# Kernel tuning notes

Hardware: AMD Instinct MI355X
Metric: run time of the kernel (lower is better)

Reference implementation:

```python
import jax, jax.numpy as jnp
import numpy as np

NUM_EXPERTS = 8
TOP_K = 2
N_EMBD = 1024
D_FFN = 2048  # 4*n_embd//top_k, already multiple of block_size=128


def setup_inputs() -> dict:
    key = jax.random.key(0)
    k1, k2, k3, k4 = jax.random.split(key, 4)
    x = jax.random.normal(k1, (4, 2048, N_EMBD), dtype=jnp.float32)
    router_w = jax.random.normal(k2, (NUM_EXPERTS, N_EMBD), dtype=jnp.float32) * 0.02
    w1 = jax.random.normal(k3, (N_EMBD, D_FFN * NUM_EXPERTS), dtype=jnp.float32) * 0.02
    w2 = jax.random.normal(k4, (D_FFN * NUM_EXPERTS, N_EMBD), dtype=jnp.float32) * 0.02
    return {"x": x, "router_w": router_w, "w1": w1, "w2": w2}


def reference(x, router_w, w1, w2):
    B, T, D = x.shape
    xf = x.reshape(B * T, D)                       # [N, d]
    N = B * T

    # Router: softmax over experts, then top-k selection and renormalization.
    logits = xf @ router_w.T                       # [N, E]
    probs = jax.nn.softmax(logits, axis=-1)
    top_v, top_i = jax.lax.top_k(probs, TOP_K)     # [N, k]
    top_v = top_v / jnp.sum(top_v, axis=-1, keepdims=True)  # norm_topk_prob=True

    # Dense [N, E] routing-weight matrix (zero for non-selected experts).
    gate = jnp.zeros((N, NUM_EXPERTS), dtype=x.dtype)
    gate = gate.at[jnp.arange(N)[:, None], top_i].set(top_v)

    w1r = w1.reshape(D, NUM_EXPERTS, D_FFN)        # expert-major column blocks
    w2r = w2.reshape(NUM_EXPERTS, D_FFN, D)

    out = jnp.zeros((N, D), dtype=x.dtype)
    for e in range(NUM_EXPERTS):
        h = jax.nn.gelu(xf @ w1r[:, e, :], approximate=False)  # [N, f]
        out = out + gate[:, e:e + 1] * (h @ w2r[e])
    return out.reshape(B, T, D)
```

## Files before the change

kernel.cpp:

```cpp
#include <hip/hip_runtime.h>
#include <hip/hip_bf16.h>
#include <cstdint>
#include <cstddef>

#define NE 8
#define N_TOK 8192
#define D_EMB 1024
#define D_FFN 2048

#define BM 128
#define BN 128
#define BK 32

typedef __attribute__((ext_vector_type(8))) short short8;
typedef __attribute__((ext_vector_type(4))) float f32x4;

__device__ __forceinline__ unsigned short f2bf(float f) {
  union { float f; unsigned int u; } c; c.f = f;
  unsigned int u = c.u;
  unsigned int r = u + 0x7FFFu + ((u >> 16) & 1u);
  return (unsigned short)(r >> 16);
}

__device__ __forceinline__ float bf2f(unsigned short u) {
  union { unsigned int u; float f; } c; c.u = ((unsigned int)u) << 16;
  return c.f;
}

__device__ __forceinline__ void gll16(const void* g, void* l) {
  __builtin_amdgcn_global_load_lds((const __attribute__((address_space(1))) void*)g,
                                   (__attribute__((address_space(3))) void*)l, 16, 0, 0);
}

__global__ __launch_bounds__(256) void router_k(const float* __restrict__ x,
                                                const float* __restrict__ rw,
                                                int* __restrict__ ti,
                                                float* __restrict__ tg,
                                                ushort* __restrict__ xb) {
  int w = threadIdx.x >> 6, lane = threadIdx.x & 63;
  int n = blockIdx.x * 4 + w;
  const float4* x4 = (const float4*)(x + (size_t)n * D_EMB);
  ushort4* xb4 = (ushort4*)(xb + (size_t)n * D_EMB);
  const float4* r4 = (const float4*)rw;
  float acc[NE];
#pragma unroll
  for (int e = 0; e < NE; ++e) acc[e] = 0.f;
#pragma unroll
  for (int c = 0; c < 4; ++c) {
    float4 xv = x4[c * 64 + lane];
    ushort4 o;
    o.x = f2bf(xv.x); o.y = f2bf(xv.y); o.z = f2bf(xv.z); o.w = f2bf(xv.w);
    xb4[c * 64 + lane] = o;
#pragma unroll
    for (int e = 0; e < NE; ++e) {
      float4 wv = r4[e * 256 + c * 64 + lane];
      acc[e] += xv.x * wv.x + xv.y * wv.y + xv.z * wv.z + xv.w * wv.w;
    }
  }
#pragma unroll
  for (int e = 0; e < NE; ++e) {
    float v = acc[e];
#pragma unroll
    for (int off = 32; off >= 1; off >>= 1) v += __shfl_xor(v, off);
    acc[e] = v;
  }
  if (lane == 0) {
    int e0 = 0; float v0 = acc[0];
#pragma unroll
    for (int e = 1; e < NE; ++e) if (acc[e] > v0) { v0 = acc[e]; e0 = e; }
    int e1 = -1; float v1 = -1e30f;
#pragma unroll
    for (int e = 0; e < NE; ++e) if (e != e0 && acc[e] > v1) { v1 = acc[e]; e1 = e; }
    float p1 = expf(v1 - v0);
    float g0 = 1.f / (1.f + p1);
    float g1 = p1 * g0;
    ti[2 * n] = e0; ti[2 * n + 1] = e1;
    tg[2 * n] = g0; tg[2 * n + 1] = g1;
  }
}

__global__ __launch_bounds__(256) void hist_k(const int* __restrict__ ti,
                                              int* __restrict__ counts) {
  __shared__ int lc[NE];
  if (threadIdx.x < NE) lc[threadIdx.x] = 0;
  __syncthreads();
  int s = blockIdx.x * 512 + threadIdx.x;
  atomicAdd(&lc[ti[s]], 1);
  atomicAdd(&lc[ti[s + 256]], 1);
  __syncthreads();
  if (threadIdx.x < NE) atomicAdd(&counts[threadIdx.x], lc[threadIdx.x]);
}

__global__ void prefix_k(const int* __restrict__ counts, int* __restrict__ bases,
                         int* __restrict__ cursor) {
  if (threadIdx.x == 0) {
    int s = 0;
    for (int e = 0; e < NE; ++e) { bases[e] = s; cursor[e] = s; s += counts[e]; }
  }
}

__global__ __launch_bounds__(256) void scatter_k(const int* __restrict__ ti,
                                                 const float* __restrict__ tg,
                                                 int* __restrict__ cursor,
                                                 int* __restrict__ tok,
                                                 float* __restrict__ gate,
                                                 int* __restrict__ inv) {
  __shared__ int lc[NE], lb[NE];
  if (threadIdx.x < NE) lc[threadIdx.x] = 0;
  __syncthreads();
  int s = blockIdx.x * 256 + threadIdx.x;
  int e = ti[s];
  float g = tg[s];
  int loc = atomicAdd(&lc[e], 1);
  __syncthreads();
  if (threadIdx.x < NE) lb[threadIdx.x] = atomicAdd(&cursor[threadIdx.x], lc[threadIdx.x]);
  __syncthreads();
  int pos = lb[e] + loc;
  tok[pos] = s >> 1;
  gate[pos] = g;
  inv[s] = pos;
}

__global__ __launch_bounds__(256) void transpose_bf_k(const float* __restrict__ src,
                                                      ushort* __restrict__ dst,
                                                      int R, int C) {
  __shared__ ushort t[32][33];
  int bx = blockIdx.x, by = blockIdx.y;
  int rl = threadIdx.x >> 3, q = threadIdx.x & 7;
  float4 v = *(const float4*)&src[(size_t)(by * 32 + rl) * C + bx * 32 + q * 4];
  t[rl][q * 4 + 0] = f2bf(v.x);
  t[rl][q * 4 + 1] = f2bf(v.y);
  t[rl][q * 4 + 2] = f2bf(v.z);
  t[rl][q * 4 + 3] = f2bf(v.w);
  __syncthreads();
  ushort4 o;
  o.x = t[q * 4 + 0][rl];
  o.y = t[q * 4 + 1][rl];
  o.z = t[q * 4 + 2][rl];
  o.w = t[q * 4 + 3][rl];
  *(ushort4*)&dst[(size_t)(bx * 32 + rl) * R + by * 32 + q * 4] = o;
}


__global__ __launch_bounds__(256) void gemm1_k(const ushort* __restrict__ xb,
                                               const ushort* __restrict__ w1t,
                                               const int* __restrict__ counts,
                                               const int* __restrict__ bases,
                                               const int* __restrict__ tok,
                                               ushort* __restrict__ h) {
  int bid = (int)blockIdx.x;
  bid = (bid & 7) * (NE * 1024 / 8) + (bid >> 3);
  int e = bid >> 10;
  int rem = bid & 1023;
  int mt = rem >> 4, nt = rem & 15;
  int count = counts[e];
  if (mt * BM >= count) return;
  int base = bases[e];

  __shared__ ushort Al[BM * BK];
  __shared__ ushort Bl[BN * BK];

  int tid = threadIdx.x;
  int w = tid >> 6, lane = tid & 63;

  const int ssw = (((lane & 3) ^ ((lane >> 3) & 3))) * 8;

  const ushort* aptr[2]; const ushort* bptr[2];
  ushort* alds[2]; ushort* blds[2];
#pragma unroll
  for (int j = 0; j < 2; ++j) {
    int rl = w * 32 + j * 16 + (lane >> 2);
    int pr = min(base + mt * BM + rl, base + count - 1);
    int t = tok[pr];
    aptr[j] = xb + (size_t)t * D_EMB + ssw;
    int c = e * D_FFN + nt * BN + rl;
    bptr[j] = w1t + (size_t)c * D_EMB + ssw;
    alds[j] = Al + (w * 32 + j * 16) * BK;
    blds[j] = Bl + (w * 32 + j * 16) * BK;
  }

  f32x4 zero = {0.f, 0.f, 0.f, 0.f};
  f32x4 acc[4][4];
#pragma unroll
  for (int i = 0; i < 4; ++i)
#pragma unroll
    for (int j = 0; j < 4; ++j) acc[i][j] = zero;

  int wm = w >> 1, wn = w & 1;
  const int rsw = ((lane >> 4) ^ (((lane & 15) >> 1) & 3)) * 8;
  const int arow = (wm * 64 + (lane & 15)) * BK + rsw;
  const int brow = (wn * 64 + (lane & 15)) * BK + rsw;

  for (int ks = 0; ks < D_EMB / BK; ++ks) {
    __syncthreads();
#pragma unroll
    for (int j = 0; j < 2; ++j) {
      gll16(aptr[j], alds[j]);
      gll16(bptr[j], blds[j]);
      aptr[j] += BK; bptr[j] += BK;
    }
    __syncthreads();
    short8 a[4], b[4];
#pragma unroll
    for (int i = 0; i < 4; ++i) a[i] = *(const short8*)&Al[arow + i * 16 * BK];
#pragma unroll
    for (int j = 0; j < 4; ++j) b[j] = *(const short8*)&Bl[brow + j * 16 * BK];
#pragma unroll
    for (int i = 0; i < 4; ++i)
#pragma unroll
      for (int j = 0; j < 4; ++j)
        acc[i][j] = __builtin_amdgcn_mfma_f32_16x16x32_bf16(a[i], b[j], acc[i][j], 0, 0, 0);
  }

  int r0 = mt * BM + wm * 64, c0 = nt * BN + wn * 64;
#pragma unroll
  for (int i = 0; i < 4; ++i) {
#pragma unroll
    for (int q = 0; q < 4; ++q) {
      int row = r0 + i * 16 + (lane >> 4) * 4 + q;
      if (row < count) {
        size_t hb = (size_t)(base + row) * D_FFN;
#pragma unroll
        for (int j = 0; j < 4; ++j) {
          float v = acc[i][j][q];
          v = 0.5f * v * (1.f + erff(v * 0.70710678118654752f));
          h[hb + c0 + j * 16 + (lane & 15)] = f2bf(v);
        }
      }
    }
  }
}

__global__ __launch_bounds__(256) void gemm2_k(const ushort* __restrict__ h,
                                               const ushort* __restrict__ w2t,
                                               const int* __restrict__ counts,
                                               const int* __restrict__ bases,
                                               const int* __restrict__ tok,
                                               const float* __restrict__ gate,
                                               ushort* __restrict__ y) {
  int bid = (int)blockIdx.x;
  bid = (bid & 7) * (NE * 512 / 8) + (bid >> 3);
  int e = bid >> 9;
  int rem = bid & 511;
  int mt = rem >> 3, nt = rem & 7;
  int count = counts[e];
  if (mt * BM >= count) return;
  int base = bases[e];

  __shared__ ushort Al[BM * BK];
  __shared__ ushort Bl[BN * BK];

  int tid = threadIdx.x;
  int w = tid >> 6, lane = tid & 63;

  const int ssw = (((lane & 3) ^ ((lane >> 3) & 3))) * 8;

  const ushort* aptr[2]; const ushort* bptr[2];
  ushort* alds[2]; ushort* blds[2];
#pragma unroll
  for (int j = 0; j < 2; ++j) {
    int rl = w * 32 + j * 16 + (lane >> 2);
    int pr = min(base + mt * BM + rl, base + count - 1);
    aptr[j] = h + (size_t)pr * D_FFN + ssw;
    int d = nt * BN + rl;
    bptr[j] = w2t + (size_t)d * (NE * D_FFN) + e * D_FFN + ssw;
    alds[j] = Al + (w * 32 + j * 16) * BK;
    blds[j] = Bl + (w * 32 + j * 16) * BK;
  }

  f32x4 zero = {0.f, 0.f, 0.f, 0.f};
  f32x4 acc[4][4];
#pragma unroll
  for (int i = 0; i < 4; ++i)
#pragma unroll
    for (int j = 0; j < 4; ++j) acc[i][j] = zero;

  int wm = w >> 1, wn = w & 1;
  const int rsw = ((lane >> 4) ^ (((lane & 15) >> 1) & 3)) * 8;
  const int arow = (wm * 64 + (lane & 15)) * BK + rsw;
  const int brow = (wn * 64 + (lane & 15)) * BK + rsw;

  for (int ks = 0; ks < D_FFN / BK; ++ks) {
    __syncthreads();
#pragma unroll
    for (int j = 0; j < 2; ++j) {
      gll16(aptr[j], alds[j]);
      gll16(bptr[j], blds[j]);
      aptr[j] += BK; bptr[j] += BK;
    }
    __syncthreads();
    short8 a[4], b[4];
#pragma unroll
    for (int i = 0; i < 4; ++i) a[i] = *(const short8*)&Al[arow + i * 16 * BK];
#pragma unroll
    for (int j = 0; j < 4; ++j) b[j] = *(const short8*)&Bl[brow + j * 16 * BK];
#pragma unroll
    for (int i = 0; i < 4; ++i)
#pragma unroll
      for (int j = 0; j < 4; ++j)
        acc[i][j] = __builtin_amdgcn_mfma_f32_16x16x32_bf16(a[i], b[j], acc[i][j], 0, 0, 0);
  }

  int r0 = mt * BM + wm * 64, c0 = nt * BN + wn * 64;
#pragma unroll
  for (int i = 0; i < 4; ++i) {
#pragma unroll
    for (int q = 0; q < 4; ++q) {
      int row = r0 + i * 16 + (lane >> 4) * 4 + q;
      if (row < count) {
        int pr = base + row;
        float g = gate[pr];
        size_t yb = (size_t)pr * D_EMB;
#pragma unroll
        for (int j = 0; j < 4; ++j) {
          y[yb + c0 + j * 16 + (lane & 15)] = f2bf(g * acc[i][j][q]);
        }
      }
    }
  }
}

__global__ __launch_bounds__(256) void combine_k(const ushort* __restrict__ y,
                                                 const int* __restrict__ inv,
                                                 float* __restrict__ out) {
  int n = blockIdx.x;
  int p0 = inv[2 * n], p1 = inv[2 * n + 1];
  const ushort4* r0 = (const ushort4*)(y + (size_t)p0 * D_EMB);
  const ushort4* r1 = (const ushort4*)(y + (size_t)p1 * D_EMB);
  float4* o = (float4*)(out + (size_t)n * D_EMB);
  int i = threadIdx.x;
  ushort4 a = r0[i], b = r1[i];
  float4 v;
  v.x = bf2f(a.x) + bf2f(b.x);
  v.y = bf2f(a.y) + bf2f(b.y);
  v.z = bf2f(a.z) + bf2f(b.z);
  v.w = bf2f(a.w) + bf2f(b.w);
  o[i] = v;
}

extern "C" void kernel_launch(void* const* d_in, const int* in_sizes, int n_in,
                              void* d_out, int out_size, void* d_ws, size_t ws_size,
                              hipStream_t stream) {
  const float* x  = (const float*)d_in[0];
  const float* rw = (const float*)d_in[1];
  const float* w1 = (const float*)d_in[2];
  const float* w2 = (const float*)d_in[3];
  float* out = (float*)d_out;

  char* ws = (char*)d_ws;
  size_t off = 0;
  auto alloc = [&](size_t bytes) {
    void* p = ws + off;
    off = (off + bytes + 255) & ~(size_t)255;
    return p;
  };
  int*    counts = (int*)alloc(32);
  int*    bases  = (int*)alloc(32);
  int*    cursor = (int*)alloc(32);
  int*    ti     = (int*)alloc((size_t)N_TOK * 2 * sizeof(int));
  float*  tg     = (float*)alloc((size_t)N_TOK * 2 * sizeof(float));
  int*    tok    = (int*)alloc((size_t)N_TOK * 2 * sizeof(int));
  float*  gate   = (float*)alloc((size_t)N_TOK * 2 * sizeof(float));
  int*    inv    = (int*)alloc((size_t)N_TOK * 2 * sizeof(int));
  ushort* xb     = (ushort*)alloc((size_t)N_TOK * D_EMB * 2);
  ushort* w1t    = (ushort*)alloc((size_t)D_EMB * NE * D_FFN * 2);
  ushort* w2t    = (ushort*)alloc((size_t)D_EMB * NE * D_FFN * 2);
  ushort* hbuf   = (ushort*)alloc((size_t)N_TOK * 2 * D_FFN * 2);
  ushort* ybuf   = (ushort*)alloc((size_t)N_TOK * 2 * D_EMB * 2);
  (void)ws_size; (void)in_sizes; (void)n_in; (void)out_size;

  hipMemsetAsync(counts, 0, 32, stream);

  router_k<<<N_TOK / 4, 256, 0, stream>>>(x, rw, ti, tg, xb);
  transpose_bf_k<<<dim3(512, 32), 256, 0, stream>>>(w1, w1t, D_EMB, NE * D_FFN);
  transpose_bf_k<<<dim3(32, 512), 256, 0, stream>>>(w2, w2t, NE * D_FFN, D_EMB);
  hist_k<<<N_TOK * 2 / 512, 256, 0, stream>>>(ti, counts);
  prefix_k<<<1, 64, 0, stream>>>(counts, bases, cursor);
  scatter_k<<<N_TOK * 2 / 256, 256, 0, stream>>>(ti, tg, cursor, tok, gate, inv);
  gemm1_k<<<NE * 64 * 16, 256, 0, stream>>>(xb, w1t, counts, bases, tok, hbuf);
  gemm2_k<<<NE * 64 * 8, 256, 0, stream>>>(hbuf, w2t, counts, bases, tok, gate, ybuf);
  combine_k<<<N_TOK, 256, 0, stream>>>(ybuf, inv, out);
}
```

Baseline: 284.6 us.

## Double-buffer LDS tiles in both expert GEMMs to overlap loads with MFMA

```diff
diff --git a/kernel.cpp b/kernel.cpp
--- a/kernel.cpp
+++ b/kernel.cpp
@@ -140,6 +140,7 @@
   o.w = t[q * 4 + 3][rl];
   *(ushort4*)&dst[(size_t)(bx * 32 + rl) * R + by * 32 + q * 4] = o;
 }
+
 
 
 __global__ __launch_bounds__(256) void gemm1_k(const ushort* __restrict__ xb,
@@ -157,8 +158,8 @@
   if (mt * BM >= count) return;
   int base = bases[e];
 
-  __shared__ ushort Al[BM * BK];
-  __shared__ ushort Bl[BN * BK];
+  __shared__ ushort Al[2][BM * BK];
+  __shared__ ushort Bl[2][BN * BK];
 
   int tid = threadIdx.x;
   int w = tid >> 6, lane = tid & 63;
@@ -166,7 +167,7 @@
   const int ssw = (((lane & 3) ^ ((lane >> 3) & 3))) * 8;
 
   const ushort* aptr[2]; const ushort* bptr[2];
-  ushort* alds[2]; ushort* blds[2];
+  int ldso[2];
 #pragma unroll
   for (int j = 0; j < 2; ++j) {
     int rl = w * 32 + j * 16 + (lane >> 2);
@@ -175,8 +176,7 @@
     aptr[j] = xb + (size_t)t * D_EMB + ssw;
     int c = e * D_FFN + nt * BN + rl;
     bptr[j] = w1t + (size_t)c * D_EMB + ssw;
-    alds[j] = Al + (w * 32 + j * 16) * BK;
-    blds[j] = Bl + (w * 32 + j * 16) * BK;
+    ldso[j] = (w * 32 + j * 16) * BK;
   }
 
   f32x4 zero = {0.f, 0.f, 0.f, 0.f};
@@ -191,26 +191,39 @@
   const int arow = (wm * 64 + (lane & 15)) * BK + rsw;
   const int brow = (wn * 64 + (lane & 15)) * BK + rsw;
 
-  for (int ks = 0; ks < D_EMB / BK; ++ks) {
-    __syncthreads();
-#pragma unroll
-    for (int j = 0; j < 2; ++j) {
-      gll16(aptr[j], alds[j]);
-      gll16(bptr[j], blds[j]);
-      aptr[j] += BK; bptr[j] += BK;
-    }
-    __syncthreads();
-    short8 a[4], b[4];
-#pragma unroll
-    for (int i = 0; i < 4; ++i) a[i] = *(const short8*)&Al[arow + i * 16 * BK];
-#pragma unroll
-    for (int j = 0; j < 4; ++j) b[j] = *(const short8*)&Bl[brow + j * 16 * BK];
-#pragma unroll
-    for (int i = 0; i < 4; ++i)
-#pragma unroll
-      for (int j = 0; j < 4; ++j)
-        acc[i][j] = __builtin_amdgcn_mfma_f32_16x16x32_bf16(a[i], b[j], acc[i][j], 0, 0, 0);
-  }
+#define STAGE1(BUF)                                         \
+  {                                                         \
+    _Pragma("unroll")                                       \
+    for (int j = 0; j < 2; ++j) {                           \
+      gll16(aptr[j], &Al[BUF][ldso[j]]);                    \
+      gll16(bptr[j], &Bl[BUF][ldso[j]]);                    \
+      aptr[j] += BK; bptr[j] += BK;                         \
+    }                                                       \
+  }
+#define COMPUTE1(BUF)                                       \
+  {                                                         \
+    short8 a[4], b[4];                                      \
+    _Pragma("unroll")                                       \
+    for (int i = 0; i < 4; ++i) a[i] = *(const short8*)&Al[BUF][arow + i * 16 * BK]; \
+    _Pragma("unroll")                                       \
+    for (int j = 0; j < 4; ++j) b[j] = *(const short8*)&Bl[BUF][brow + j * 16 * BK]; \
+    _Pragma("unroll")                                       \
+    for (int i = 0; i < 4; ++i)                             \
+      _Pragma("unroll")                                     \
+      for (int j = 0; j < 4; ++j)                           \
+        acc[i][j] = __builtin_amdgcn_mfma_f32_16x16x32_bf16(a[i], b[j], acc[i][j], 0, 0, 0); \
+  }
+
+  STAGE1(0);
+  __syncthreads();
+  for (int ks = 0; ks < (D_EMB / BK) - 2; ks += 2) {
+    STAGE1(1); COMPUTE1(0); __syncthreads();
+    STAGE1(0); COMPUTE1(1); __syncthreads();
+  }
+  STAGE1(1); COMPUTE1(0); __syncthreads();
+  COMPUTE1(1);
+#undef STAGE1
+#undef COMPUTE1
 
   int r0 = mt * BM + wm * 64, c0 = nt * BN + wn * 64;
 #pragma unroll
@@ -247,8 +260,8 @@
   if (mt * BM >= count) return;
   int base = bases[e];
 
-  __shared__ ushort Al[BM * BK];
-  __shared__ ushort Bl[BN * BK];
+  __shared__ ushort Al[2][BM * BK];
+  __shared__ ushort Bl[2][BN * BK];
 
   int tid = threadIdx.x;
   int w = tid >> 6, lane = tid & 63;
@@ -256,7 +269,7 @@
   const int ssw = (((lane & 3) ^ ((lane >> 3) & 3))) * 8;
 
   const ushort* aptr[2]; const ushort* bptr[2];
-  ushort* alds[2]; ushort* blds[2];
+  int ldso[2];
 #pragma unroll
   for (int j = 0; j < 2; ++j) {
     int rl = w * 32 + j * 16 + (lane >> 2);
@@ -264,8 +277,7 @@
     aptr[j] = h + (size_t)pr * D_FFN + ssw;
     int d = nt * BN + rl;
     bptr[j] = w2t + (size_t)d * (NE * D_FFN) + e * D_FFN + ssw;
-    alds[j] = Al + (w * 32 + j * 16) * BK;
-    blds[j] = Bl + (w * 32 + j * 16) * BK;
+    ldso[j] = (w * 32 + j * 16) * BK;
   }
 
   f32x4 zero = {0.f, 0.f, 0.f, 0.f};
@@ -280,26 +292,39 @@
   const int arow = (wm * 64 + (lane & 15)) * BK + rsw;
   const int brow = (wn * 64 + (lane & 15)) * BK + rsw;
 
-  for (int ks = 0; ks < D_FFN / BK; ++ks) {
-    __syncthreads();
-#pragma unroll
-    for (int j = 0; j < 2; ++j) {
-      gll16(aptr[j], alds[j]);
-      gll16(bptr[j], blds[j]);
-      aptr[j] += BK; bptr[j] += BK;
-    }
-    __syncthreads();
-    short8 a[4], b[4];
-#pragma unroll
-    for (int i = 0; i < 4; ++i) a[i] = *(const short8*)&Al[arow + i * 16 * BK];
-#pragma unroll
-    for (int j = 0; j < 4; ++j) b[j] = *(const short8*)&Bl[brow + j * 16 * BK];
-#pragma unroll
-    for (int i = 0; i < 4; ++i)
-#pragma unroll
-      for (int j = 0; j < 4; ++j)
-        acc[i][j] = __builtin_amdgcn_mfma_f32_16x16x32_bf16(a[i], b[j], acc[i][j], 0, 0, 0);
-  }
+#define STAGE2(BUF)                                         \
+  {                                                         \
+    _Pragma("unroll")                                       \
+    for (int j = 0; j < 2; ++j) {                           \
+      gll16(aptr[j], &Al[BUF][ldso[j]]);                    \
+      gll16(bptr[j], &Bl[BUF][ldso[j]]);                    \
+      aptr[j] += BK; bptr[j] += BK;                         \
+    }                                                       \
+  }
+#define COMPUTE2(BUF)                                       \
+  {                                                         \
+    short8 a[4], b[4];                                      \
+    _Pragma("unroll")                                       \
+    for (int i = 0; i < 4; ++i) a[i] = *(const short8*)&Al[BUF][arow + i * 16 * BK]; \
+    _Pragma("unroll")                                       \
+    for (int j = 0; j < 4; ++j) b[j] = *(const short8*)&Bl[BUF][brow + j * 16 * BK]; \
+    _Pragma("unroll")                                       \
+    for (int i = 0; i < 4; ++i)                             \
+      _Pragma("unroll")                                     \
+      for (int j = 0; j < 4; ++j)                           \
+        acc[i][j] = __builtin_amdgcn_mfma_f32_16x16x32_bf16(a[i], b[j], acc[i][j], 0, 0, 0); \
+  }
+
+  STAGE2(0);
+  __syncthreads();
+  for (int ks = 0; ks < (D_FFN / BK) - 2; ks += 2) {
+    STAGE2(1); COMPUTE2(0); __syncthreads();
+    STAGE2(0); COMPUTE2(1); __syncthreads();
+  }
+  STAGE2(1); COMPUTE2(0); __syncthreads();
+  COMPUTE2(1);
+#undef STAGE2
+#undef COMPUTE2
 
   int r0 = mt * BM + wm * 64, c0 = nt * BN + wn * 64;
 #pragma unroll
```

After: 303.5 us. +6.6%, slower.

## Rewrite expert GEMMs as 256x256 double-buffered 8-wave tiles with interleaved MFMA

Applied to the files above, without the earlier changes.

```diff
diff --git a/kernel.cpp b/kernel.cpp
--- a/kernel.cpp
+++ b/kernel.cpp
@@ -7,10 +7,6 @@
 #define N_TOK 8192
 #define D_EMB 1024
 #define D_FFN 2048
-
-#define BM 128
-#define BN 128
-#define BK 32
 
 typedef __attribute__((ext_vector_type(8))) short short8;
 typedef __attribute__((ext_vector_type(4))) float f32x4;
@@ -31,6 +27,8 @@
   __builtin_amdgcn_global_load_lds((const __attribute__((address_space(1))) void*)g,
                                    (__attribute__((address_space(3))) void*)l, 16, 0, 0);
 }
+
+#define SB() __builtin_amdgcn_sched_barrier(0)
 
 __global__ __launch_bounds__(256) void router_k(const float* __restrict__ x,
                                                 const float* __restrict__ rw,
@@ -142,79 +140,117 @@
 }
 
 
-__global__ __launch_bounds__(256) void gemm1_k(const ushort* __restrict__ xb,
-                                               const ushort* __restrict__ w1t,
-                                               const int* __restrict__ counts,
-                                               const int* __restrict__ bases,
-                                               const int* __restrict__ tok,
-                                               ushort* __restrict__ h) {
+#define RD_A(dst, BASE, ROFF)                                              \
+  { _Pragma("unroll") for (int f_ = 0; f_ < 4; ++f_)                       \
+    _Pragma("unroll") for (int kk_ = 0; kk_ < 2; ++kk_) {                  \
+      int row_ = (ROFF) + f_ * 16 + (lane & 15);                           \
+      int s_ = kk_ * 4 + (lane >> 4);                                      \
+      dst[f_][kk_] = *(const short8*)&(BASE)[row_ * 64 + ((s_ ^ (row_ & 7)) * 8)]; \
+    } }
+
+#define RD_B(dst, BASE, ROFF)                                              \
+  { _Pragma("unroll") for (int g_ = 0; g_ < 2; ++g_)                       \
+    _Pragma("unroll") for (int kk_ = 0; kk_ < 2; ++kk_) {                  \
+      int row_ = (ROFF) + g_ * 16 + (lane & 15);                           \
+      int s_ = kk_ * 4 + (lane >> 4);                                      \
+      dst[g_][kk_] = *(const short8*)&(BASE)[row_ * 64 + ((s_ ^ (row_ & 7)) * 8)]; \
+    } }
+
+#define MFMA_Q(QR, QC, FA, FB)                                             \
+  { __builtin_amdgcn_s_setprio(1);                                        \
+    _Pragma("unroll") for (int f_ = 0; f_ < 4; ++f_)                       \
+    _Pragma("unroll") for (int g_ = 0; g_ < 2; ++g_)                       \
+    _Pragma("unroll") for (int kk_ = 0; kk_ < 2; ++kk_)                    \
+      acc[(QR) * 4 + f_][(QC) * 2 + g_] = __builtin_amdgcn_mfma_f32_16x16x32_bf16( \
+          FA[f_][kk_], FB[g_][kk_], acc[(QR) * 4 + f_][(QC) * 2 + g_], 0, 0, 0);   \
+    __builtin_amdgcn_s_setprio(0); }
+
+#define STAGE(AD, BD)                                                      \
+  { _Pragma("unroll") for (int r_ = 0; r_ < 4; ++r_) {                     \
+      gll16(aP[r_], (AD) + (r_ * 64 + wv * 8) * 64); aP[r_] += 64;         \
+      gll16(bP[r_], (BD) + (r_ * 64 + wv * 8) * 64); bP[r_] += 64;         \
+    } }
+
+#define TILE(CURA, CURB, NXTA, NXTB, DONXT)                                \
+  {                                                                \
+    if (DONXT) { STAGE(NXTA, NXTB); }                                      \
+    RD_A(fA1, CURA, wm * 128 + 64); RD_B(fB1, CURB, wn * 64 + 32);         \
+    MFMA_Q(0, 0, fA0, fB0);                                                \
+    SB(); __builtin_amdgcn_s_barrier(); SB();                              \
+                                                                   \
+    MFMA_Q(0, 1, fA0, fB1);                                                \
+    SB(); __builtin_amdgcn_s_barrier(); SB();                              \
+                                                                   \
+    MFMA_Q(1, 0, fA1, fB0);                                                \
+    SB(); __builtin_amdgcn_s_barrier(); SB();                              \
+                                                                   \
+    MFMA_Q(1, 1, fA1, fB1);                                                \
+    if (DONXT) { asm volatile("s_waitcnt vmcnt(0)" ::: "memory"); SB(); }  \
+    SB(); __builtin_amdgcn_s_barrier(); SB();                              \
+    if (DONXT) { RD_A(fA0, NXTA, wm * 128); RD_B(fB0, NXTB, wn * 64); }    \
+  }
+
+__global__ __launch_bounds__(512, 2) void gemm1_k(const ushort* __restrict__ xb,
+                                                  const ushort* __restrict__ w1t,
+                                                  const int* __restrict__ counts,
+                                                  const int* __restrict__ bases,
+                                                  const int* __restrict__ tok,
+                                                  ushort* __restrict__ h) {
   int bid = (int)blockIdx.x;
-  bid = (bid & 7) * (NE * 1024 / 8) + (bid >> 3);
-  int e = bid >> 10;
-  int rem = bid & 1023;
-  int mt = rem >> 4, nt = rem & 15;
+  bid = (bid & 7) * 256 + (bid >> 3);
+  int e = bid >> 8;
+  int rem = bid & 255;
+  int mt = rem >> 3, nt = rem & 7;
   int count = counts[e];
-  if (mt * BM >= count) return;
+  if (mt * 256 >= count) return;
   int base = bases[e];
 
-  __shared__ ushort Al[BM * BK];
-  __shared__ ushort Bl[BN * BK];
+  extern __shared__ ushort smem[];
+  ushort* A0_ = smem;
+  ushort* A1_ = smem + 16384;
+  ushort* B0_ = smem + 32768;
+  ushort* B1_ = smem + 49152;
 
   int tid = threadIdx.x;
-  int w = tid >> 6, lane = tid & 63;
-
-  const int ssw = (((lane & 3) ^ ((lane >> 3) & 3))) * 8;
-
-  const ushort* aptr[2]; const ushort* bptr[2];
-  ushort* alds[2]; ushort* blds[2];
-#pragma unroll
-  for (int j = 0; j < 2; ++j) {
-    int rl = w * 32 + j * 16 + (lane >> 2);
-    int pr = min(base + mt * BM + rl, base + count - 1);
+  int wv = tid >> 6, lane = tid & 63;
+  int wm = wv >> 2, wn = wv & 3;
+  const int swc = ((tid & 7) ^ ((tid >> 3) & 7)) * 8;
+
+  const ushort* aP[4]; const ushort* bP[4];
+#pragma unroll
+  for (int r = 0; r < 4; ++r) {
+    int row = mt * 256 + r * 64 + (tid >> 3);
+    int pr = min(base + row, base + count - 1);
     int t = tok[pr];
-    aptr[j] = xb + (size_t)t * D_EMB + ssw;
-    int c = e * D_FFN + nt * BN + rl;
-    bptr[j] = w1t + (size_t)c * D_EMB + ssw;
-    alds[j] = Al + (w * 32 + j * 16) * BK;
-    blds[j] = Bl + (w * 32 + j * 16) * BK;
+    aP[r] = xb + (size_t)t * D_EMB + swc;
+    int cB = e * D_FFN + nt * 256 + r * 64 + (tid >> 3);
+    bP[r] = w1t + (size_t)cB * D_EMB + swc;
   }
 
   f32x4 zero = {0.f, 0.f, 0.f, 0.f};
-  f32x4 acc[4][4];
-#pragma unroll
-  for (int i = 0; i < 4; ++i)
+  f32x4 acc[8][4];
+#pragma unroll
+  for (int i = 0; i < 8; ++i)
 #pragma unroll
     for (int j = 0; j < 4; ++j) acc[i][j] = zero;
 
-  int wm = w >> 1, wn = w & 1;
-  const int rsw = ((lane >> 4) ^ (((lane & 15) >> 1) & 3)) * 8;
-  const int arow = (wm * 64 + (lane & 15)) * BK + rsw;
-  const int brow = (wn * 64 + (lane & 15)) * BK + rsw;
-
-  for (int ks = 0; ks < D_EMB / BK; ++ks) {
-    __syncthreads();
-#pragma unroll
-    for (int j = 0; j < 2; ++j) {
-      gll16(aptr[j], alds[j]);
-      gll16(bptr[j], blds[j]);
-      aptr[j] += BK; bptr[j] += BK;
-    }
-    __syncthreads();
-    short8 a[4], b[4];
-#pragma unroll
-    for (int i = 0; i < 4; ++i) a[i] = *(const short8*)&Al[arow + i * 16 * BK];
-#pragma unroll
-    for (int j = 0; j < 4; ++j) b[j] = *(const short8*)&Bl[brow + j * 16 * BK];
-#pragma unroll
-    for (int i = 0; i < 4; ++i)
-#pragma unroll
-      for (int j = 0; j < 4; ++j)
-        acc[i][j] = __builtin_amdgcn_mfma_f32_16x16x32_bf16(a[i], b[j], acc[i][j], 0, 0, 0);
-  }
-
-  int r0 = mt * BM + wm * 64, c0 = nt * BN + wn * 64;
-#pragma unroll
-  for (int i = 0; i < 4; ++i) {
+  short8 fA0[4][2], fA1[4][2], fB0[2][2], fB1[2][2];
+
+  STAGE(A0_, B0_);
+  asm volatile("s_waitcnt vmcnt(0)" ::: "memory"); SB();
+  __builtin_amdgcn_s_barrier(); SB();
+  RD_A(fA0, A0_, wm * 128); RD_B(fB0, B0_, wn * 64);
+
+  const int NT = D_EMB / 64;
+  for (int tp = 0; tp < NT / 2; ++tp) {
+    TILE(A0_, B0_, A1_, B1_, 1);
+    int dn = (tp != NT / 2 - 1);
+    TILE(A1_, B1_, A0_, B0_, dn);
+  }
+
+  int r0 = mt * 256 + wm * 128, c0 = nt * 256 + wn * 64;
+#pragma unroll
+  for (int i = 0; i < 8; ++i) {
 #pragma unroll
     for (int q = 0; q < 4; ++q) {
       int row = r0 + i * 16 + (lane >> 4) * 4 + q;
@@ -231,79 +267,66 @@
   }
 }
 
-__global__ __launch_bounds__(256) void gemm2_k(const ushort* __restrict__ h,
-                                               const ushort* __restrict__ w2t,
-                                               const int* __restrict__ counts,
-                                               const int* __restrict__ bases,
-                                               const int* __restrict__ tok,
-                                               const float* __restrict__ gate,
-                                               ushort* __restrict__ y) {
+__global__ __launch_bounds__(512, 2) void gemm2_k(const ushort* __restrict__ h,
+                                                  const ushort* __restrict__ w2t,
+                                                  const int* __restrict__ counts,
+                                                  const int* __restrict__ bases,
+                                                  const float* __restrict__ gate,
+                                                  ushort* __restrict__ y) {
   int bid = (int)blockIdx.x;
-  bid = (bid & 7) * (NE * 512 / 8) + (bid >> 3);
-  int e = bid >> 9;
-  int rem = bid & 511;
-  int mt = rem >> 3, nt = rem & 7;
+  bid = (bid & 7) * 128 + (bid >> 3);
+  int e = bid >> 7;
+  int rem = bid & 127;
+  int mt = rem >> 2, nt = rem & 3;
   int count = counts[e];
-  if (mt * BM >= count) return;
+  if (mt * 256 >= count) return;
   int base = bases[e];
 
-  __shared__ ushort Al[BM * BK];
-  __shared__ ushort Bl[BN * BK];
+  extern __shared__ ushort smem[];
+  ushort* A0_ = smem;
+  ushort* A1_ = smem + 16384;
+  ushort* B0_ = smem + 32768;
+  ushort* B1_ = smem + 49152;
 
   int tid = threadIdx.x;
-  int w = tid >> 6, lane = tid & 63;
-
-  const int ssw = (((lane & 3) ^ ((lane >> 3) & 3))) * 8;
-
-  const ushort* aptr[2]; const ushort* bptr[2];
-  ushort* alds[2]; ushort* blds[2];
-#pragma unroll
-  for (int j = 0; j < 2; ++j) {
-    int rl = w * 32 + j * 16 + (lane >> 2);
-    int pr = min(base + mt * BM + rl, base + count - 1);
-    aptr[j] = h + (size_t)pr * D_FFN + ssw;
-    int d = nt * BN + rl;
-    bptr[j] = w2t + (size_t)d * (NE * D_FFN) + e * D_FFN + ssw;
-    alds[j] = Al + (w * 32 + j * 16) * BK;
-    blds[j] = Bl + (w * 32 + j * 16) * BK;
+  int wv = tid >> 6, lane = tid & 63;
+  int wm = wv >> 2, wn = wv & 3;
+  const int swc = ((tid & 7) ^ ((tid >> 3) & 7)) * 8;
+
+  const ushort* aP[4]; const ushort* bP[4];
+#pragma unroll
+  for (int r = 0; r < 4; ++r) {
+    int row = mt * 256 + r * 64 + (tid >> 3);
+    int pr = min(base + row, base + count - 1);
+    aP[r] = h + (size_t)pr * D_FFN + swc;
+    int cB = nt * 256 + r * 64 + (tid >> 3);
+    bP[r] = w2t + (size_t)cB * (NE * D_FFN) + e * D_FFN + swc;
   }
 
   f32x4 zero = {0.f, 0.f, 0.f, 0.f};
-  f32x4 acc[4][4];
-#pragma unroll
-  for (int i = 0; i < 4; ++i)
+  f32x4 acc[8][4];
+#pragma unroll
+  for (int i = 0; i < 8; ++i)
 #pragma unroll
     for (int j = 0; j < 4; ++j) acc[i][j] = zero;
 
-  int wm = w >> 1, wn = w & 1;
-  const int rsw = ((lane >> 4) ^ (((lane & 15) >> 1) & 3)) * 8;
-  const int arow = (wm * 64 + (lane & 15)) * BK + rsw;
-  const int brow = (wn * 64 + (lane & 15)) * BK + rsw;
-
-  for (int ks = 0; ks < D_FFN / BK; ++ks) {
-    __syncthreads();
-#pragma unroll
-    for (int j = 0; j < 2; ++j) {
-      gll16(aptr[j], alds[j]);
-      gll16(bptr[j], blds[j]);
-      aptr[j] += BK; bptr[j] += BK;
-    }
-    __syncthreads();
-    short8 a[4], b[4];
-#pragma unroll
-    for (int i = 0; i < 4; ++i) a[i] = *(const short8*)&Al[arow + i * 16 * BK];
-#pragma unroll
-    for (int j = 0; j < 4; ++j) b[j] = *(const short8*)&Bl[brow + j * 16 * BK];
-#pragma unroll
-    for (int i = 0; i < 4; ++i)
-#pragma unroll
-      for (int j = 0; j < 4; ++j)
-        acc[i][j] = __builtin_amdgcn_mfma_f32_16x16x32_bf16(a[i], b[j], acc[i][j], 0, 0, 0);
-  }
-
-  int r0 = mt * BM + wm * 64, c0 = nt * BN + wn * 64;
-#pragma unroll
-  for (int i = 0; i < 4; ++i) {
+  short8 fA0[4][2], fA1[4][2], fB0[2][2], fB1[2][2];
+
+  STAGE(A0_, B0_);
+  asm volatile("s_waitcnt vmcnt(0)" ::: "memory"); SB();
+  __builtin_amdgcn_s_barrier(); SB();
+  RD_A(fA0, A0_, wm * 128); RD_B(fB0, B0_, wn * 64);
+
+  const int NT = D_FFN / 64;
+  for (int tp = 0; tp < NT / 2; ++tp) {
+    TILE(A0_, B0_, A1_, B1_, 1);
+    int dn = (tp != NT / 2 - 1);
+    TILE(A1_, B1_, A0_, B0_, dn);
+  }
+
+  int r0 = mt * 256 + wm * 128, c0 = nt * 256 + wn * 64;
+#pragma unroll
+  for (int i = 0; i < 8; ++i) {
 #pragma unroll
     for (int q = 0; q < 4; ++q) {
       int row = r0 + i * 16 + (lane >> 4) * 4 + q;
@@ -369,6 +392,9 @@
   ushort* ybuf   = (ushort*)alloc((size_t)N_TOK * 2 * D_EMB * 2);
   (void)ws_size; (void)in_sizes; (void)n_in; (void)out_size;
 
+  hipFuncSetAttribute((const void*)gemm1_k, hipFuncAttributeMaxDynamicSharedMemorySize, 131072);
+  hipFuncSetAttribute((const void*)gemm2_k, hipFuncAttributeMaxDynamicSharedMemorySize, 131072);
+
   hipMemsetAsync(counts, 0, 32, stream);
 
   router_k<<<N_TOK / 4, 256, 0, stream>>>(x, rw, ti, tg, xb);
@@ -377,7 +403,7 @@
   hist_k<<<N_TOK * 2 / 512, 256, 0, stream>>>(ti, counts);
   prefix_k<<<1, 64, 0, stream>>>(counts, bases, cursor);
   scatter_k<<<N_TOK * 2 / 256, 256, 0, stream>>>(ti, tg, cursor, tok, gate, inv);
-  gemm1_k<<<NE * 64 * 16, 256, 0, stream>>>(xb, w1t, counts, bases, tok, hbuf);
-  gemm2_k<<<NE * 64 * 8, 256, 0, stream>>>(hbuf, w2t, counts, bases, tok, gate, ybuf);
+  gemm1_k<<<NE * 256, 512, 131072, stream>>>(xb, w1t, counts, bases, tok, hbuf);
+  gemm2_k<<<NE * 128, 512, 131072, stream>>>(hbuf, w2t, counts, bases, gate, ybuf);
   combine_k<<<N_TOK, 256, 0, stream>>>(ybuf, inv, out);
 }
```

After: 413.8 us. 1.45x slower.

## Double-buffer LDS with BK=64 and async-load pipelining in expert GEMMs

Applied to the files above, without the earlier changes.

```diff
diff --git a/kernel.cpp b/kernel.cpp
--- a/kernel.cpp
+++ b/kernel.cpp
@@ -10,7 +10,7 @@
 
 #define BM 128
 #define BN 128
-#define BK 32
+#define BK 64
 
 typedef __attribute__((ext_vector_type(8))) short short8;
 typedef __attribute__((ext_vector_type(4))) float f32x4;
@@ -31,6 +31,10 @@
   __builtin_amdgcn_global_load_lds((const __attribute__((address_space(1))) void*)g,
                                    (__attribute__((address_space(3))) void*)l, 16, 0, 0);
 }
+
+#define SB() __builtin_amdgcn_sched_barrier(0)
+#define VW(N) { asm volatile("s_waitcnt vmcnt(" #N ")" ::: "memory"); SB(); }
+#define BAR() { SB(); __builtin_amdgcn_s_barrier(); SB(); }
 
 __global__ __launch_bounds__(256) void router_k(const float* __restrict__ x,
                                                 const float* __restrict__ rw,
@@ -141,6 +145,39 @@
   *(ushort4*)&dst[(size_t)(bx * 32 + rl) * R + by * 32 + q * 4] = o;
 }
 
+
+#define STAGEK(BUF)                                                        \
+  { _Pragma("unroll") for (int r_ = 0; r_ < 4; ++r_) {                     \
+      gll16(aP[r_], &Al[BUF][r_ * 2048 + w * 512]); aP[r_] += BK;          \
+      gll16(bP[r_], &Bl[BUF][r_ * 2048 + w * 512]); bP[r_] += BK;          \
+    } }
+
+#define COMPUTEK(BUF)                                                      \
+  { short8 a[4], b[4];                                                     \
+    _Pragma("unroll") for (int i = 0; i < 4; ++i)                          \
+      a[i] = *(const short8*)&Al[BUF][(wm * 64 + i * 16 + l15) * 64 + q0]; \
+    _Pragma("unroll") for (int j = 0; j < 4; ++j)                          \
+      b[j] = *(const short8*)&Bl[BUF][(wn * 64 + j * 16 + l15) * 64 + q0]; \
+    _Pragma("unroll") for (int i = 0; i < 4; ++i)                          \
+      _Pragma("unroll") for (int j = 0; j < 4; ++j)                        \
+        acc[i][j] = __builtin_amdgcn_mfma_f32_16x16x32_bf16(a[i], b[j], acc[i][j], 0, 0, 0); \
+    _Pragma("unroll") for (int i = 0; i < 4; ++i)                          \
+      a[i] = *(const short8*)&Al[BUF][(wm * 64 + i * 16 + l15) * 64 + (q0 ^ 32)]; \
+    _Pragma("unroll") for (int j = 0; j < 4; ++j)                          \
+      b[j] = *(const short8*)&Bl[BUF][(wn * 64 + j * 16 + l15) * 64 + (q0 ^ 32)]; \
+    _Pragma("unroll") for (int i = 0; i < 4; ++i)                          \
+      _Pragma("unroll") for (int j = 0; j < 4; ++j)                        \
+        acc[i][j] = __builtin_amdgcn_mfma_f32_16x16x32_bf16(a[i], b[j], acc[i][j], 0, 0, 0); \
+  }
+
+#define KLOOP(NT)                                                          \
+  STAGEK(0);                                                               \
+  for (int ks = 0; ks < (NT) - 2; ks += 2) {                               \
+    STAGEK(1); VW(8); BAR(); COMPUTEK(0); BAR();                           \
+    STAGEK(0); VW(8); BAR(); COMPUTEK(1); BAR();                           \
+  }                                                                        \
+  STAGEK(1); VW(8); BAR(); COMPUTEK(0); BAR();                             \
+  VW(0); BAR(); COMPUTEK(1);
 
 __global__ __launch_bounds__(256) void gemm1_k(const ushort* __restrict__ xb,
                                                const ushort* __restrict__ w1t,
@@ -157,26 +194,25 @@
   if (mt * BM >= count) return;
   int base = bases[e];
 
-  __shared__ ushort Al[BM * BK];
-  __shared__ ushort Bl[BN * BK];
+  __shared__ ushort Al[2][BM * BK];
+  __shared__ ushort Bl[2][BN * BK];
 
   int tid = threadIdx.x;
   int w = tid >> 6, lane = tid & 63;
-
-  const int ssw = (((lane & 3) ^ ((lane >> 3) & 3))) * 8;
-
-  const ushort* aptr[2]; const ushort* bptr[2];
-  ushort* alds[2]; ushort* blds[2];
-#pragma unroll
-  for (int j = 0; j < 2; ++j) {
-    int rl = w * 32 + j * 16 + (lane >> 2);
-    int pr = min(base + mt * BM + rl, base + count - 1);
+  const int l15 = lane & 15;
+  const int q0 = (((lane >> 4) ^ (lane & 7))) * 8;
+
+  const int swc = (((tid & 7) ^ ((tid >> 3) & 7))) * 8;
+
+  const ushort* aP[4]; const ushort* bP[4];
+#pragma unroll
+  for (int r = 0; r < 4; ++r) {
+    int R = r * 32 + (tid >> 3);
+    int pr = min(base + mt * BM + R, base + count - 1);
     int t = tok[pr];
-    aptr[j] = xb + (size_t)t * D_EMB + ssw;
-    int c = e * D_FFN + nt * BN + rl;
-    bptr[j] = w1t + (size_t)c * D_EMB + ssw;
-    alds[j] = Al + (w * 32 + j * 16) * BK;
-    blds[j] = Bl + (w * 32 + j * 16) * BK;
+    aP[r] = xb + (size_t)t * D_EMB + swc;
+    int cB = e * D_FFN + nt * BN + R;
+    bP[r] = w1t + (size_t)cB * D_EMB + swc;
   }
 
   f32x4 zero = {0.f, 0.f, 0.f, 0.f};
@@ -187,30 +223,8 @@
     for (int j = 0; j < 4; ++j) acc[i][j] = zero;
 
   int wm = w >> 1, wn = w & 1;
-  const int rsw = ((lane >> 4) ^ (((lane & 15) >> 1) & 3)) * 8;
-  const int arow = (wm * 64 + (lane & 15)) * BK + rsw;
-  const int brow = (wn * 64 + (lane & 15)) * BK + rsw;
-
-  for (int ks = 0; ks < D_EMB / BK; ++ks) {
-    __syncthreads();
-#pragma unroll
-    for (int j = 0; j < 2; ++j) {
-      gll16(aptr[j], alds[j]);
-      gll16(bptr[j], blds[j]);
-      aptr[j] += BK; bptr[j] += BK;
-    }
-    __syncthreads();
-    short8 a[4], b[4];
-#pragma unroll
-    for (int i = 0; i < 4; ++i) a[i] = *(const short8*)&Al[arow + i * 16 * BK];
-#pragma unroll
-    for (int j = 0; j < 4; ++j) b[j] = *(const short8*)&Bl[brow + j * 16 * BK];
-#pragma unroll
-    for (int i = 0; i < 4; ++i)
-#pragma unroll
-      for (int j = 0; j < 4; ++j)
-        acc[i][j] = __builtin_amdgcn_mfma_f32_16x16x32_bf16(a[i], b[j], acc[i][j], 0, 0, 0);
-  }
+
+  KLOOP(D_EMB / BK);
 
   int r0 = mt * BM + wm * 64, c0 = nt * BN + wn * 64;
 #pragma unroll
@@ -224,7 +238,7 @@
         for (int j = 0; j < 4; ++j) {
           float v = acc[i][j][q];
           v = 0.5f * v * (1.f + erff(v * 0.70710678118654752f));
-          h[hb + c0 + j * 16 + (lane & 15)] = f2bf(v);
+          h[hb + c0 + j * 16 + l15] = f2bf(v);
         }
       }
     }
@@ -235,7 +249,6 @@
                                                const ushort* __restrict__ w2t,
                                                const int* __restrict__ counts,
                                                const int* __restrict__ bases,
-                                               const int* __restrict__ tok,
                                                const float* __restrict__ gate,
                                                ushort* __restrict__ y) {
   int bid = (int)blockIdx.x;
@@ -247,25 +260,23 @@
   if (mt * BM >= count) return;
   int base = bases[e];
 
-  __shared__ ushort Al[BM * BK];
-  __shared__ ushort Bl[BN * BK];
+  __shared__ ushort Al[2][BM * BK];
+  __shared__ ushort Bl[2][BN * BK];
 
   int tid = threadIdx.x;
   int w = tid >> 6, lane = tid & 63;
-
-  const int ssw = (((lane & 3) ^ ((lane >> 3) & 3))) * 8;
-
-  const ushort* aptr[2]; const ushort* bptr[2];
-  ushort* alds[2]; ushort* blds[2];
-#pragma unroll
-  for (int j = 0; j < 2; ++j) {
-    int rl = w * 32 + j * 16 + (lane >> 2);
-    int pr = min(base + mt * BM + rl, base + count - 1);
-    aptr[j] = h + (size_t)pr * D_FFN + ssw;
-    int d = nt * BN + rl;
-    bptr[j] = w2t + (size_t)d * (NE * D_FFN) + e * D_FFN + ssw;
-    alds[j] = Al + (w * 32 + j * 16) * BK;
-    blds[j] = Bl + (w * 32 + j * 16) * BK;
+  const int l15 = lane & 15;
+  const int q0 = (((lane >> 4) ^ (lane & 7))) * 8;
+  const int swc = (((tid & 7) ^ ((tid >> 3) & 7))) * 8;
+
+  const ushort* aP[4]; const ushort* bP[4];
+#pragma unroll
+  for (int r = 0; r < 4; ++r) {
+    int R = r * 32 + (tid >> 3);
+    int pr = min(base + mt * BM + R, base + count - 1);
+    aP[r] = h + (size_t)pr * D_FFN + swc;
+    int d = nt * BN + R;
+    bP[r] = w2t + (size_t)d * (NE * D_FFN) + e * D_FFN + swc;
   }
 
   f32x4 zero = {0.f, 0.f, 0.f, 0.f};
@@ -276,30 +287,8 @@
     for (int j = 0; j < 4; ++j) acc[i][j] = zero;
 
   int wm = w >> 1, wn = w & 1;
-  const int rsw = ((lane >> 4) ^ (((lane & 15) >> 1) & 3)) * 8;
-  const int arow = (wm * 64 + (lane & 15)) * BK + rsw;
-  const int brow = (wn * 64 + (lane & 15)) * BK + rsw;
-
-  for (int ks = 0; ks < D_FFN / BK; ++ks) {
-    __syncthreads();
-#pragma unroll
-    for (int j = 0; j < 2; ++j) {
-      gll16(aptr[j], alds[j]);
-      gll16(bptr[j], blds[j]);
-      aptr[j] += BK; bptr[j] += BK;
-    }
-    __syncthreads();
-    short8 a[4], b[4];
-#pragma unroll
-    for (int i = 0; i < 4; ++i) a[i] = *(const short8*)&Al[arow + i * 16 * BK];
-#pragma unroll
-    for (int j = 0; j < 4; ++j) b[j] = *(const short8*)&Bl[brow + j * 16 * BK];
-#pragma unroll
-    for (int i = 0; i < 4; ++i)
-#pragma unroll
-      for (int j = 0; j < 4; ++j)
-        acc[i][j] = __builtin_amdgcn_mfma_f32_16x16x32_bf16(a[i], b[j], acc[i][j], 0, 0, 0);
-  }
+
+  KLOOP(D_FFN / BK);
 
   int r0 = mt * BM + wm * 64, c0 = nt * BN + wn * 64;
 #pragma unroll
@@ -313,7 +302,7 @@
         size_t yb = (size_t)pr * D_EMB;
 #pragma unroll
         for (int j = 0; j < 4; ++j) {
-          y[yb + c0 + j * 16 + (lane & 15)] = f2bf(g * acc[i][j][q]);
+          y[yb + c0 + j * 16 + l15] = f2bf(g * acc[i][j][q]);
         }
       }
     }
@@ -378,6 +367,6 @@
   prefix_k<<<1, 64, 0, stream>>>(counts, bases, cursor);
   scatter_k<<<N_TOK * 2 / 256, 256, 0, stream>>>(ti, tg, cursor, tok, gate, inv);
   gemm1_k<<<NE * 64 * 16, 256, 0, stream>>>(xb, w1t, counts, bases, tok, hbuf);
-  gemm2_k<<<NE * 64 * 8, 256, 0, stream>>>(hbuf, w2t, counts, bases, tok, gate, ybuf);
+  gemm2_k<<<NE * 64 * 8, 256, 0, stream>>>(hbuf, w2t, counts, bases, gate, ybuf);
   combine_k<<<N_TOK, 256, 0, stream>>>(ybuf, inv, out);
 }
```

Measured after the change: 312.0 us. 9.6% more time.
